# Kernel tuning notes

Hardware: AMD Instinct MI355X
Metric: run time of the kernel (lower is better)

Reference implementation:

```python
import jax, jax.numpy as jnp
import numpy as np

B, T, D = 1, 2048, 1024
HQ, HKV, HD = 16, 4, 64
G = HQ // HKV
E, TOPK, F = 8, 2, 2752
LB = 0.01
SCALE = HD ** -0.5


def setup_inputs() -> dict:
    key = jax.random.key(0)
    ks = jax.random.split(key, 12)
    s = 0.02
    return {
        "x": jax.random.normal(ks[0], (B, T, D), jnp.float32),
        "g1": jnp.ones((D,), jnp.float32),
        "g2": jnp.ones((D,), jnp.float32),
        "wq": jax.random.normal(ks[1], (D, HQ * HD), jnp.float32) * s,
        "wk": jax.random.normal(ks[2], (D, HKV * HD), jnp.float32) * s,
        "wv": jax.random.normal(ks[3], (D, HKV * HD), jnp.float32) * s,
        "wo": jax.random.normal(ks[4], (D, D), jnp.float32) * s,
        "gate_w": jax.random.normal(ks[5], (D, E), jnp.float32) * s,
        "we_gate": jax.random.normal(ks[6], (E, D, F), jnp.float32) * s,
        "we_up": jax.random.normal(ks[7], (E, D, F), jnp.float32) * s,
        "we_down": jax.random.normal(ks[8], (E, F, D), jnp.float32) * s,
    }


def _rmsnorm(x, g, eps=1e-6):
    return x * g * jax.lax.rsqrt(jnp.mean(x * x, axis=-1, keepdims=True) + eps)


def _rope(q, k):
    # q: [B,HQ,T,HD], k: [B,HKV,T,HD]; standard rotate-half RoPE
    pos = jnp.arange(T, dtype=jnp.float32)
    inv_freq = 1.0 / (10000.0 ** (jnp.arange(0, HD, 2, dtype=jnp.float32) / HD))
    ang = pos[:, None] * inv_freq[None, :]                  # [T, HD/2]
    cos = jnp.concatenate([jnp.cos(ang), jnp.cos(ang)], -1)  # [T, HD]
    sin = jnp.concatenate([jnp.sin(ang), jnp.sin(ang)], -1)

    def rot_half(x):
        x1, x2 = jnp.split(x, 2, axis=-1)
        return jnp.concatenate([-x2, x1], axis=-1)

    def apply(x):
        return x * cos + rot_half(x) * sin
    return apply(q), apply(k)


def _attention(x, g1, wq, wk, wv, wo):
    h = _rmsnorm(x, g1)
    q = (h @ wq).reshape(B, T, HQ, HD).transpose(0, 2, 1, 3)   # [B,HQ,T,HD]
    k = (h @ wk).reshape(B, T, HKV, HD).transpose(0, 2, 1, 3)  # [B,HKV,T,HD]
    v = (h @ wv).reshape(B, T, HKV, HD).transpose(0, 2, 1, 3)
    q, k = _rope(q, k)
    qg = q.reshape(B, HKV, G, T, HD)
    # grouped scores without materializing repeated K/V
    scores = jnp.einsum('bkgtd,bksd->bkgts', qg, k) * SCALE     # [B,HKV,G,T,T]
    causal = jnp.tril(jnp.ones((T, T), bool))
    scores = jnp.where(causal, scores, jnp.float32(-jnp.inf))
    w = jax.nn.softmax(scores, axis=-1)
    o = jnp.einsum('bkgts,bksd->bkgtd', w, v)                  # [B,HKV,G,T,HD]
    o = o.reshape(B, HQ, T, HD).transpose(0, 2, 1, 3).reshape(B, T, D)
    return o @ wo


def _moe(x, g2, gate_w, we_gate, we_up, we_down):
    h = _rmsnorm(x, g2).reshape(B * T, D)                      # [N,D]
    N = B * T
    logits = h @ gate_w                                        # [N,E]
    probs = jax.nn.softmax(logits, axis=-1)
    topv, topi = jax.lax.top_k(probs, TOPK)                    # [N,TOPK]
    topv = topv / (topv.sum(-1, keepdims=True) + 1e-8)
    # dense combine weights [N,E]: same math as masked per-expert dispatch
    combine = jnp.zeros((N, E), h.dtype).at[jnp.arange(N)[:, None], topi].add(topv)
    gh = jnp.einsum('nd,edf->enf', h, we_gate)
    up = jnp.einsum('nd,edf->enf', h, we_up)
    y = jnp.einsum('enf,efd->end', jax.nn.silu(gh) * up, we_down)
    out = jnp.einsum('end,ne->nd', y, combine).reshape(B, T, D)
    # load-balancing aux loss
    frac = jnp.zeros((E,), probs.dtype).at[topi.reshape(-1)].add(1.0) / (N * TOPK)
    load = probs.mean(axis=0)
    aux = LB * E * jnp.sum(frac * load)
    return out, aux


def reference(x, g1, g2, wq, wk, wv, wo, gate_w, we_gate, we_up, we_down):
    x = x + _attention(x, g1, wq, wk, wv, wo)
    moe_out, aux = _moe(x, g2, gate_w, we_gate, we_up, we_down)
    x = x + moe_out
    return x, aux
```

## Files before the change

kernel.cpp:

```cpp
#include <hip/hip_runtime.h>
#include <cstdint>

typedef __attribute__((ext_vector_type(8))) short short8;
typedef __attribute__((ext_vector_type(4))) float floatx4;
typedef __attribute__((ext_vector_type(4))) unsigned short ushort4v;
typedef unsigned short ushort;

#define T_LEN 2048
#define D_DIM 1024
#define HQn 16
#define HKVn 4
#define NE 8
#define FF 2752
#define NTOK 2048
#define NSLOT 4096
#define ATT_SCALE 0.125f
#define GATE_TPB 16

__device__ inline ushort f2bf(float f) {
  union { float f; unsigned int i; } v; v.f = f;
  unsigned int r = v.i + 0x7fffu + ((v.i >> 16) & 1u);
  return (ushort)(r >> 16);
}
__device__ inline float bf2f(ushort h) {
  union { unsigned int i; float f; } v; v.i = ((unsigned int)h) << 16;
  return v.f;
}
__device__ inline void split8(const float* v, short8& hi, short8& lo) {
#pragma unroll
  for (int i = 0; i < 8; i++) {
    ushort h = f2bf(v[i]);
    hi[i] = (short)h;
    lo[i] = (short)f2bf(v[i] - bf2f(h));
  }
}
__device__ inline floatx4 mfma16(short8 a, short8 b, floatx4 c) {
  return __builtin_amdgcn_mfma_f32_16x16x32_bf16(a, b, c, 0, 0, 0);
}
#define DMA16(g, l)                                                              \
  __builtin_amdgcn_global_load_lds((const __attribute__((address_space(1))) void*)(g), \
                                   (__attribute__((address_space(3))) void*)(l), 16, 0, 0)

__global__ __launch_bounds__(256) void k_cvtT(const float* __restrict__ src,
                                              ushort* __restrict__ dst, int R, int C) {
  __shared__ float tile[32][33];
  size_t sb = (size_t)blockIdx.z * R * C;
  const float* s = src + sb;
  ushort* d = dst + sb;
  int r0 = blockIdx.y * 32, c0 = blockIdx.x * 32;
  int tc = threadIdx.x & 31, tr = threadIdx.x >> 5;
#pragma unroll
  for (int i = 0; i < 4; i++)
    tile[tr + i * 8][tc] = s[(size_t)(r0 + tr + i * 8) * C + c0 + tc];
  __syncthreads();
#pragma unroll
  for (int i = 0; i < 4; i++) {
    int cc = tr + i * 8;
    d[(size_t)(c0 + cc) * R + r0 + tc] = f2bf(tile[tc][cc]);
  }
}

__global__ __launch_bounds__(256) void k_cvtT2(const float* __restrict__ src,
                                               ushort* __restrict__ dh,
                                               ushort* __restrict__ dl, int R, int C) {
  __shared__ float tile[32][33];
  int r0 = blockIdx.y * 32, c0 = blockIdx.x * 32;
  int tc = threadIdx.x & 31, tr = threadIdx.x >> 5;
#pragma unroll
  for (int i = 0; i < 4; i++)
    tile[tr + i * 8][tc] = src[(size_t)(r0 + tr + i * 8) * C + c0 + tc];
  __syncthreads();
#pragma unroll
  for (int i = 0; i < 4; i++) {
    int cc = tr + i * 8;
    float v = tile[tc][cc];
    ushort h = f2bf(v);
    dh[(size_t)(c0 + cc) * R + r0 + tc] = h;
    dl[(size_t)(c0 + cc) * R + r0 + tc] = f2bf(v - bf2f(h));
  }
}

__global__ __launch_bounds__(256) void k_rmsnorm2(const float* __restrict__ x,
                                                  const float* __restrict__ g,
                                                  ushort* __restrict__ oh,
                                                  ushort* __restrict__ ol) {
  int row = blockIdx.x;
  int t = threadIdx.x;
  const float4* x4 = (const float4*)(x + (size_t)row * D_DIM);
  float4 v = x4[t];
  float ss = v.x * v.x + v.y * v.y + v.z * v.z + v.w * v.w;
#pragma unroll
  for (int off = 32; off; off >>= 1) ss += __shfl_xor(ss, off, 64);
  __shared__ float red[4];
  if ((t & 63) == 0) red[t >> 6] = ss;
  __syncthreads();
  float tot = red[0] + red[1] + red[2] + red[3];
  float sc = rsqrtf(tot * (1.0f / D_DIM) + 1e-6f);
  const float4* g4 = (const float4*)g;
  float4 gv = g4[t];
  float vals[4] = {v.x * gv.x * sc, v.y * gv.y * sc, v.z * gv.z * sc, v.w * gv.w * sc};
  ushort4v h4, l4;
#pragma unroll
  for (int i = 0; i < 4; i++) {
    ushort h = f2bf(vals[i]);
    h4[i] = h;
    l4[i] = f2bf(vals[i] - bf2f(h));
  }
  *(ushort4v*)(oh + (size_t)row * D_DIM + t * 4) = h4;
  *(ushort4v*)(ol + (size_t)row * D_DIM + t * 4) = l4;
}

__global__ __launch_bounds__(256) void k_sgemm(const ushort* __restrict__ Ahg,
                                               const ushort* __restrict__ Alg,
                                               const ushort* __restrict__ Bhg,
                                               const ushort* __restrict__ Blg,
                                               float* __restrict__ C,
                                               const float* __restrict__ res,
                                               int N, int K) {
  __shared__ __align__(16) ushort Ah[2048], Al[2048], Bh[4096], Bl[4096];
  int tid = threadIdx.x;
  int m0 = blockIdx.y * 64, n0 = blockIdx.x * 128;
  int wave = tid >> 6, lane = tid & 63, quad = lane >> 4, l15 = lane & 15;
  int wm = (wave >> 1) * 32, wn = (wave & 1) * 64;
  floatx4 acc[2][4];
#pragma unroll
  for (int i = 0; i < 2; i++)
#pragma unroll
    for (int j = 0; j < 4; j++) acc[i][j] = (floatx4){0.f, 0.f, 0.f, 0.f};
  const ushort* src[6];
  ushort* dst[6];
  int srow = lane >> 2;
  int kc = ((lane & 3) ^ ((lane >> 3) & 3)) * 8;
#pragma unroll
  for (int j = 0; j < 6; j++) {
    int c = wave * 6 + j;
    if (c < 4) {
      src[j] = Ahg + (size_t)(m0 + c * 16 + srow) * K + kc;
      dst[j] = Ah + c * 512;
    } else if (c < 8) {
      src[j] = Alg + (size_t)(m0 + (c - 4) * 16 + srow) * K + kc;
      dst[j] = Al + (c - 4) * 512;
    } else if (c < 16) {
      src[j] = Bhg + (size_t)(n0 + (c - 8) * 16 + srow) * K + kc;
      dst[j] = Bh + (c - 8) * 512;
    } else {
      src[j] = Blg + (size_t)(n0 + (c - 16) * 16 + srow) * K + kc;
      dst[j] = Bl + (c - 16) * 512;
    }
  }
  for (int k0 = 0; k0 < K; k0 += 32) {
#pragma unroll
    for (int j = 0; j < 6; j++) DMA16(src[j] + k0, dst[j]);
    __syncthreads();
    short8 ah[2], al[2], bh[4], bl[4];
#pragma unroll
    for (int mt = 0; mt < 2; mt++) {
      int ar = wm + mt * 16 + l15;
      int sw = (quad ^ ((ar >> 1) & 3)) * 8;
      ah[mt] = *(short8*)&Ah[ar * 32 + sw];
      al[mt] = *(short8*)&Al[ar * 32 + sw];
    }
#pragma unroll
    for (int nt = 0; nt < 4; nt++) {
      int br = wn + nt * 16 + l15;
      int sw = (quad ^ ((br >> 1) & 3)) * 8;
      bh[nt] = *(short8*)&Bh[br * 32 + sw];
      bl[nt] = *(short8*)&Bl[br * 32 + sw];
    }
#pragma unroll
    for (int mt = 0; mt < 2; mt++)
#pragma unroll
      for (int nt = 0; nt < 4; nt++) {
        acc[mt][nt] = mfma16(ah[mt], bh[nt], acc[mt][nt]);
        acc[mt][nt] = mfma16(ah[mt], bl[nt], acc[mt][nt]);
        acc[mt][nt] = mfma16(al[mt], bh[nt], acc[mt][nt]);
      }
    __syncthreads();
  }
#pragma unroll
  for (int mt = 0; mt < 2; mt++) {
    int row = m0 + wm + mt * 16 + quad * 4;
#pragma unroll
    for (int nt = 0; nt < 4; nt++) {
      int col = n0 + wn + nt * 16 + l15;
#pragma unroll
      for (int r = 0; r < 4; r++) {
        float v = acc[mt][nt][r];
        if (res) v += res[(size_t)(row + r) * N + col];
        C[(size_t)(row + r) * N + col] = v;
      }
    }
  }
}

__global__ __launch_bounds__(256) void k_rope_cvt(const float* __restrict__ qkvf,
                                                  float* __restrict__ qbh,
                                                  float* __restrict__ kbh) {
  int t = blockIdx.x;
  const float* row = qkvf + (size_t)t * 1536;
  for (int it = threadIdx.x; it < (HQn + HKVn) * 32; it += 256) {
    int hh = it >> 5, i = it & 31;
    float inv = powf(10000.0f, -(float)i / 32.0f);
    float ang = (float)t * inv;
    float c = cosf(ang), s = sinf(ang);
    const float* p;
    float* dst;
    if (hh < HQn) {
      p = row + hh * 64;
      dst = qbh + ((size_t)hh * T_LEN + t) * 64;
    } else {
      int h2 = hh - HQn;
      p = row + 1024 + h2 * 64;
      dst = kbh + ((size_t)h2 * T_LEN + t) * 64;
    }
    float a = p[i], b = p[i + 32];
    dst[i] = a * c - b * s;
    dst[i + 32] = b * c + a * s;
  }
}

__global__ __launch_bounds__(256) void k_vT(const float* __restrict__ qkvf,
                                            float* __restrict__ vbt) {
  __shared__ float tile[32][33];
  int t0 = blockIdx.x * 32;
  int dh = blockIdx.y;
  int col0 = 1280 + dh * 32;
  int tc = threadIdx.x & 31, tr = threadIdx.x >> 5;
#pragma unroll
  for (int i = 0; i < 4; i++)
    tile[tr + i * 8][tc] = qkvf[(size_t)(t0 + tr + i * 8) * 1536 + col0 + tc];
  __syncthreads();
#pragma unroll
  for (int i = 0; i < 4; i++) {
    int dd = tr + i * 8;
    vbt[(size_t)(dh * 32 + dd) * T_LEN + t0 + tc] = tile[tc][dd];
  }
}

__global__ __launch_bounds__(256) void k_attn(const float* __restrict__ qbh,
                                              const float* __restrict__ kbh,
                                              const float* __restrict__ vbt,
                                              ushort* __restrict__ obh,
                                              ushort* __restrict__ obl) {
  __shared__ ushort Kh[64][72], Kl[64][72], Vh[64][72], Vl[64][72];
  __shared__ ushort Psh[4][16][72], Psl[4][16][72];
  int qh = blockIdx.y, kvh = qh >> 2;
  int r0 = blockIdx.x * 64;
  int tid = threadIdx.x, wave = tid >> 6, lane = tid & 63;
  int quad = lane >> 4, l15 = lane & 15;
#pragma unroll
  for (int it = 0; it < 2; it++) {
    int c = tid + it * 256;
    int row = c >> 3, col = (c & 7) * 8;
    float va[8];
    short8 h8, l8;
    const float* src = qbh + ((size_t)qh * T_LEN + r0 + row) * 64 + col;
    *(float4*)(va) = *(const float4*)(src);
    *(float4*)(va + 4) = *(const float4*)(src + 4);
    split8(va, h8, l8);
    *(short8*)&Kh[row][col] = h8;
    *(short8*)&Kl[row][col] = l8;
  }
  __syncthreads();
  short8 aqh0 = *(short8*)&Kh[wave * 16 + l15][quad * 8];
  short8 aqh1 = *(short8*)&Kh[wave * 16 + l15][32 + quad * 8];
  short8 aql0 = *(short8*)&Kl[wave * 16 + l15][quad * 8];
  short8 aql1 = *(short8*)&Kl[wave * 16 + l15][32 + quad * 8];
  floatx4 oacc[4];
#pragma unroll
  for (int nt = 0; nt < 4; nt++) oacc[nt] = (floatx4){0.f, 0.f, 0.f, 0.f};
  float mrun[4], lrun[4];
#pragma unroll
  for (int r = 0; r < 4; r++) { mrun[r] = -INFINITY; lrun[r] = 0.f; }
  int cq = r0 >> 6;
  for (int cc = 0; cc <= cq; cc++) {
    __syncthreads();
#pragma unroll
    for (int it = 0; it < 2; it++) {
      int c = tid + it * 256;
      int row = c >> 3, col = (c & 7) * 8;
      float va[8];
      short8 h8, l8;
      const float* ks = kbh + ((size_t)kvh * T_LEN + cc * 64 + row) * 64 + col;
      *(float4*)(va) = *(const float4*)(ks);
      *(float4*)(va + 4) = *(const float4*)(ks + 4);
      split8(va, h8, l8);
      *(short8*)&Kh[row][col] = h8;
      *(short8*)&Kl[row][col] = l8;
      const float* vs = vbt + ((size_t)(kvh * 64 + row)) * T_LEN + cc * 64 + col;
      *(float4*)(va) = *(const float4*)(vs);
      *(float4*)(va + 4) = *(const float4*)(vs + 4);
      split8(va, h8, l8);
      *(short8*)&Vh[row][col] = h8;
      *(short8*)&Vl[row][col] = l8;
    }
    __syncthreads();
    floatx4 s[4];
#pragma unroll
    for (int nt = 0; nt < 4; nt++) {
      short8 bh0 = *(short8*)&Kh[nt * 16 + l15][quad * 8];
      short8 bh1 = *(short8*)&Kh[nt * 16 + l15][32 + quad * 8];
      short8 bl0 = *(short8*)&Kl[nt * 16 + l15][quad * 8];
      short8 bl1 = *(short8*)&Kl[nt * 16 + l15][32 + quad * 8];
      floatx4 z = (floatx4){0.f, 0.f, 0.f, 0.f};
      z = mfma16(aqh0, bh0, z);
      z = mfma16(aqh1, bh1, z);
      z = mfma16(aqh0, bl0, z);
      z = mfma16(aqh1, bl1, z);
      z = mfma16(aql0, bh0, z);
      z = mfma16(aql1, bh1, z);
      s[nt] = z;
    }
    int rowg0 = r0 + wave * 16 + quad * 4;
#pragma unroll
    for (int nt = 0; nt < 4; nt++) {
      int colg = cc * 64 + nt * 16 + l15;
#pragma unroll
      for (int r = 0; r < 4; r++) {
        float v = s[nt][r] * ATT_SCALE;
        s[nt][r] = (colg > rowg0 + r) ? -INFINITY : v;
      }
    }
    float mnew[4], alpha[4], psum[4];
#pragma unroll
    for (int r = 0; r < 4; r++) {
      float mx = fmaxf(fmaxf(s[0][r], s[1][r]), fmaxf(s[2][r], s[3][r]));
#pragma unroll
      for (int off = 1; off < 16; off <<= 1) mx = fmaxf(mx, __shfl_xor(mx, off, 64));
      mnew[r] = fmaxf(mrun[r], mx);
      psum[r] = 0.f;
    }
#pragma unroll
    for (int nt = 0; nt < 4; nt++)
#pragma unroll
      for (int r = 0; r < 4; r++) {
        float p = __expf(s[nt][r] - mnew[r]);
        s[nt][r] = p;
        psum[r] += p;
      }
#pragma unroll
    for (int r = 0; r < 4; r++) {
      float ps = psum[r];
#pragma unroll
      for (int off = 1; off < 16; off <<= 1) ps += __shfl_xor(ps, off, 64);
      alpha[r] = __expf(mrun[r] - mnew[r]);
      lrun[r] = lrun[r] * alpha[r] + ps;
      mrun[r] = mnew[r];
    }
#pragma unroll
    for (int nt = 0; nt < 4; nt++)
#pragma unroll
      for (int r = 0; r < 4; r++) oacc[nt][r] *= alpha[r];
#pragma unroll
    for (int nt = 0; nt < 4; nt++)
#pragma unroll
      for (int r = 0; r < 4; r++) {
        float p = s[nt][r];
        ushort ph = f2bf(p);
        Psh[wave][quad * 4 + r][nt * 16 + l15] = ph;
        Psl[wave][quad * 4 + r][nt * 16 + l15] = f2bf(p - bf2f(ph));
      }
    short8 aph0 = *(short8*)&Psh[wave][l15][quad * 8];
    short8 aph1 = *(short8*)&Psh[wave][l15][32 + quad * 8];
    short8 apl0 = *(short8*)&Psl[wave][l15][quad * 8];
    short8 apl1 = *(short8*)&Psl[wave][l15][32 + quad * 8];
#pragma unroll
    for (int nt = 0; nt < 4; nt++) {
      short8 bvh0 = *(short8*)&Vh[nt * 16 + l15][quad * 8];
      short8 bvh1 = *(short8*)&Vh[nt * 16 + l15][32 + quad * 8];
      short8 bvl0 = *(short8*)&Vl[nt * 16 + l15][quad * 8];
      short8 bvl1 = *(short8*)&Vl[nt * 16 + l15][32 + quad * 8];
      oacc[nt] = mfma16(aph0, bvh0, oacc[nt]);
      oacc[nt] = mfma16(aph1, bvh1, oacc[nt]);
      oacc[nt] = mfma16(aph0, bvl0, oacc[nt]);
      oacc[nt] = mfma16(aph1, bvl1, oacc[nt]);
      oacc[nt] = mfma16(apl0, bvh0, oacc[nt]);
      oacc[nt] = mfma16(apl1, bvh1, oacc[nt]);
    }
  }
#pragma unroll
  for (int nt = 0; nt < 4; nt++)
#pragma unroll
    for (int r = 0; r < 4; r++) {
      int rowg = r0 + wave * 16 + quad * 4 + r;
      float v = oacc[nt][r] / lrun[r];
      ushort h = f2bf(v);
      size_t idx = (size_t)rowg * D_DIM + qh * 64 + nt * 16 + l15;
      obh[idx] = h;
      obl[idx] = f2bf(v - bf2f(h));
    }
}

__global__ __launch_bounds__(256) void k_gate(const float* __restrict__ x1,
                                              const float* __restrict__ g2,
                                              const float* __restrict__ gw,
                                              int* __restrict__ counts,
                                              int* __restrict__ ids,
                                              float* __restrict__ wts,
                                              float* __restrict__ load_sum) {
  __shared__ float lsum[NE];
  __shared__ int lcount[NE];
  __shared__ int lbase[NE];
  __shared__ int ltok[GATE_TPB * 2];
  __shared__ int lexp[GATE_TPB * 2];
  __shared__ float lwt[GATE_TPB * 2];
  int tid = threadIdx.x, wave = tid >> 6, lane = tid & 63;
  if (tid < NE) { lsum[tid] = 0.f; lcount[tid] = 0; }
  __syncthreads();
  int t0 = blockIdx.x * GATE_TPB;
#pragma unroll
  for (int tt = 0; tt < GATE_TPB / 4; tt++) {
    int tloc = tt * 4 + wave;
    int token = t0 + tloc;
    const float* xp = x1 + (size_t)token * D_DIM;
    float acc[NE] = {};
    float ss = 0.f;
    for (int d = lane; d < D_DIM; d += 64) {
      float xv = xp[d];
      ss += xv * xv;
      float hv = xv * g2[d];
#pragma unroll
      for (int e = 0; e < NE; e++) acc[e] += hv * gw[d * NE + e];
    }
#pragma unroll
    for (int off = 32; off; off >>= 1) ss += __shfl_xor(ss, off, 64);
#pragma unroll
    for (int e = 0; e < NE; e++)
#pragma unroll
      for (int off = 32; off; off >>= 1) acc[e] += __shfl_xor(acc[e], off, 64);
    if (lane == 0) {
      float sc = rsqrtf(ss * (1.0f / D_DIM) + 1e-6f);
      float mx = -1e30f;
#pragma unroll
      for (int e = 0; e < NE; e++) { acc[e] *= sc; mx = fmaxf(mx, acc[e]); }
      float p[NE], sum = 0.f;
#pragma unroll
      for (int e = 0; e < NE; e++) { p[e] = expf(acc[e] - mx); sum += p[e]; }
#pragma unroll
      for (int e = 0; e < NE; e++) p[e] /= sum;
      int i1 = 0;
#pragma unroll
      for (int e = 1; e < NE; e++) if (acc[e] > acc[i1]) i1 = e;
      int i2 = (i1 == 0) ? 1 : 0;
#pragma unroll
      for (int e = 0; e < NE; e++) if (e != i1 && acc[e] > acc[i2]) i2 = e;
      float denom = p[i1] + p[i2] + 1e-8f;
      int slot = tloc * 2;
      lexp[slot] = i1; ltok[slot] = token; lwt[slot] = p[i1] / denom;
      lexp[slot + 1] = i2; ltok[slot + 1] = token; lwt[slot + 1] = p[i2] / denom;
      atomicAdd(&lcount[i1], 1);
      atomicAdd(&lcount[i2], 1);
#pragma unroll
      for (int e = 0; e < NE; e++) atomicAdd(&lsum[e], p[e]);
    }
  }
  __syncthreads();
  if (tid < NE) {
    lbase[tid] = atomicAdd(&counts[tid], lcount[tid]);
    atomicAdd(&load_sum[tid], lsum[tid]);
    lcount[tid] = 0;
  }
  __syncthreads();
  if (tid < GATE_TPB * 2) {
    int e = lexp[tid];
    int off = atomicAdd(&lcount[e], 1);
    int pos = lbase[e] + off;
    ids[e * NTOK + pos] = ltok[tid];
    wts[e * NTOK + pos] = lwt[tid];
  }
}

__global__ void k_offsets(const int* __restrict__ counts, int* __restrict__ offsets) {
  if (threadIdx.x == 0 && blockIdx.x == 0) {
    int s = 0;
    for (int e = 0; e < NE; e++) { offsets[e] = s; s += counts[e]; }
  }
}

__global__ __launch_bounds__(256) void k_moe_gateup(const ushort* __restrict__ h,
                                                    const ushort* __restrict__ wgT,
                                                    const ushort* __restrict__ wuT,
                                                    const int* __restrict__ ids,
                                                    const float* __restrict__ wts,
                                                    const int* __restrict__ counts,
                                                    const int* __restrict__ offsets,
                                                    ushort* __restrict__ act) {
  int e = blockIdx.z;
  int cnt = counts[e];
  int m0 = blockIdx.y * 128;
  if (m0 >= cnt) return;
  int n0 = blockIdx.x * 64;
  __shared__ __align__(16) ushort As[4096], Bg[2048], Bu[2048];
  __shared__ int toks[128];
  __shared__ float wrow[128];
  int tid = threadIdx.x;
  if (tid < 128) {
    int mm = m0 + tid;
    toks[tid] = (mm < cnt) ? ids[e * NTOK + mm] : 0;
    wrow[tid] = (mm < cnt) ? wts[e * NTOK + mm] : 0.f;
  }
  __syncthreads();
  int wave = tid >> 6, lane = tid & 63, quad = lane >> 4, l15 = lane & 15;
  int wm = (wave >> 1) * 64, wn = (wave & 1) * 32;
  const ushort* Wg = wgT + (size_t)e * FF * D_DIM;
  const ushort* Wu = wuT + (size_t)e * FF * D_DIM;
  const ushort* src[4];
  ushort* dst[4];
  int srow = lane >> 2;
  int kc = ((lane & 3) ^ ((lane >> 3) & 3)) * 8;
#pragma unroll
  for (int j = 0; j < 4; j++) {
    int c = wave * 4 + j;
    if (c < 8) {
      src[j] = h + (size_t)toks[c * 16 + srow] * D_DIM + kc;
      dst[j] = As + c * 512;
    } else if (c < 12) {
      src[j] = Wg + (size_t)(n0 + (c - 8) * 16 + srow) * D_DIM + kc;
      dst[j] = Bg + (c - 8) * 512;
    } else {
      src[j] = Wu + (size_t)(n0 + (c - 12) * 16 + srow) * D_DIM + kc;
      dst[j] = Bu + (c - 12) * 512;
    }
  }
  floatx4 accg[4][2], accu[4][2];
#pragma unroll
  for (int i = 0; i < 4; i++)
#pragma unroll
    for (int j = 0; j < 2; j++) {
      accg[i][j] = (floatx4){0.f, 0.f, 0.f, 0.f};
      accu[i][j] = (floatx4){0.f, 0.f, 0.f, 0.f};
    }
  for (int k0 = 0; k0 < D_DIM; k0 += 32) {
#pragma unroll
    for (int j = 0; j < 4; j++) DMA16(src[j] + k0, dst[j]);
    __syncthreads();
    short8 aF[4], bgF[2], buF[2];
#pragma unroll
    for (int mt = 0; mt < 4; mt++) {
      int ar = wm + mt * 16 + l15;
      int sw = (quad ^ ((ar >> 1) & 3)) * 8;
      aF[mt] = *(short8*)&As[ar * 32 + sw];
    }
#pragma unroll
    for (int nt = 0; nt < 2; nt++) {
      int br = wn + nt * 16 + l15;
      int sw = (quad ^ ((br >> 1) & 3)) * 8;
      bgF[nt] = *(short8*)&Bg[br * 32 + sw];
      buF[nt] = *(short8*)&Bu[br * 32 + sw];
    }
#pragma unroll
    for (int mt = 0; mt < 4; mt++)
#pragma unroll
      for (int nt = 0; nt < 2; nt++) {
        accg[mt][nt] = mfma16(aF[mt], bgF[nt], accg[mt][nt]);
        accu[mt][nt] = mfma16(aF[mt], buF[nt], accu[mt][nt]);
      }
    __syncthreads();
  }
  int aoff = offsets[e];
#pragma unroll
  for (int mt = 0; mt < 4; mt++) {
    int mrow = wm + mt * 16 + quad * 4;
#pragma unroll
    for (int nt = 0; nt < 2; nt++) {
      int col = n0 + wn + nt * 16 + l15;
#pragma unroll
      for (int r = 0; r < 4; r++) {
        int ml = mrow + r;
        if (m0 + ml < cnt) {
          float g = accg[mt][nt][r];
          float u = accu[mt][nt][r];
          float sil = g / (1.f + __expf(-g));
          act[(size_t)(aoff + m0 + ml) * FF + col] = f2bf(sil * u * wrow[ml]);
        }
      }
    }
  }
}

__global__ __launch_bounds__(256) void k_moe_down(const ushort* __restrict__ act,
                                                  const ushort* __restrict__ wdT,
                                                  const int* __restrict__ ids,
                                                  const int* __restrict__ counts,
                                                  const int* __restrict__ offsets,
                                                  float* __restrict__ moe_acc) {
  int e = blockIdx.z & 7;
  int kh = blockIdx.z >> 3;
  int cnt = counts[e];
  int m0 = blockIdx.y * 128;
  if (m0 >= cnt) return;
  int n0 = blockIdx.x * 128;
  __shared__ __align__(16) ushort As[4096], Bs[4096];
  __shared__ int toks[128];
  int tid = threadIdx.x;
  if (tid < 128) {
    int mm = m0 + tid;
    toks[tid] = (mm < cnt) ? ids[e * NTOK + mm] : 0;
  }
  __syncthreads();
  int wave = tid >> 6, lane = tid & 63, quad = lane >> 4, l15 = lane & 15;
  int wm = (wave >> 1) * 64, wn = (wave & 1) * 64;
  int aoff = offsets[e];
  const ushort* Wd = wdT + (size_t)e * D_DIM * FF;
  const ushort* src[4];
  ushort* dst[4];
  int srow = lane >> 2;
  int kc = ((lane & 3) ^ ((lane >> 3) & 3)) * 8;
#pragma unroll
  for (int j = 0; j < 4; j++) {
    int c = wave * 4 + j;
    if (c < 8) {
      src[j] = act + (size_t)(aoff + m0 + c * 16 + srow) * FF + kc;
      dst[j] = As + c * 512;
    } else {
      src[j] = Wd + (size_t)(n0 + (c - 8) * 16 + srow) * FF + kc;
      dst[j] = Bs + (c - 8) * 512;
    }
  }
  floatx4 acc[4][4];
#pragma unroll
  for (int i = 0; i < 4; i++)
#pragma unroll
    for (int j = 0; j < 4; j++) acc[i][j] = (floatx4){0.f, 0.f, 0.f, 0.f};
  int kbeg = kh * 1376;
  for (int k0 = kbeg; k0 < kbeg + 1376; k0 += 32) {
#pragma unroll
    for (int j = 0; j < 4; j++) DMA16(src[j] + k0, dst[j]);
    __syncthreads();
    short8 aF[4], bF[4];
#pragma unroll
    for (int mt = 0; mt < 4; mt++) {
      int ar = wm + mt * 16 + l15;
      int sw = (quad ^ ((ar >> 1) & 3)) * 8;
      aF[mt] = *(short8*)&As[ar * 32 + sw];
    }
#pragma unroll
    for (int nt = 0; nt < 4; nt++) {
      int br = wn + nt * 16 + l15;
      int sw = (quad ^ ((br >> 1) & 3)) * 8;
      bF[nt] = *(short8*)&Bs[br * 32 + sw];
    }
#pragma unroll
    for (int mt = 0; mt < 4; mt++)
#pragma unroll
      for (int nt = 0; nt < 4; nt++) acc[mt][nt] = mfma16(aF[mt], bF[nt], acc[mt][nt]);
    __syncthreads();
  }
#pragma unroll
  for (int mt = 0; mt < 4; mt++) {
    int mrow = wm + mt * 16 + quad * 4;
#pragma unroll
    for (int nt = 0; nt < 4; nt++) {
      int col = n0 + wn + nt * 16 + l15;
#pragma unroll
      for (int r = 0; r < 4; r++) {
        int ml = mrow + r;
        if (m0 + ml < cnt)
          atomicAdd(&moe_acc[(size_t)toks[ml] * D_DIM + col], acc[mt][nt][r]);
      }
    }
  }
}

__global__ __launch_bounds__(256) void k_add(const float* __restrict__ a,
                                             const float* __restrict__ b,
                                             float* __restrict__ o) {
  int i = blockIdx.x * 256 + threadIdx.x;
  float4 va = ((const float4*)a)[i];
  float4 vb = ((const float4*)b)[i];
  float4 vo;
  vo.x = va.x + vb.x; vo.y = va.y + vb.y; vo.z = va.z + vb.z; vo.w = va.w + vb.w;
  ((float4*)o)[i] = vo;
}

__global__ void k_aux(const int* __restrict__ counts, const float* __restrict__ load_sum,
                      float* __restrict__ out_aux) {
  if (threadIdx.x == 0 && blockIdx.x == 0) {
    float s = 0.f;
    for (int e = 0; e < NE; e++)
      s += ((float)counts[e] / (float)NSLOT) * (load_sum[e] / (float)NTOK);
    *out_aux = 0.01f * (float)NE * s;
  }
}

extern "C" void kernel_launch(void* const* d_in, const int* in_sizes, int n_in,
                              void* d_out, int out_size, void* d_ws, size_t ws_size,
                              hipStream_t stream) {
  const float* x = (const float*)d_in[0];
  const float* g1 = (const float*)d_in[1];
  const float* g2 = (const float*)d_in[2];
  const float* wq = (const float*)d_in[3];
  const float* wk = (const float*)d_in[4];
  const float* wv = (const float*)d_in[5];
  const float* wo = (const float*)d_in[6];
  const float* gate_w = (const float*)d_in[7];
  const float* we_gate = (const float*)d_in[8];
  const float* we_up = (const float*)d_in[9];
  const float* we_down = (const float*)d_in[10];
  float* out = (float*)d_out;

  char* w = (char*)d_ws;
  size_t o = 0;
  auto alloc = [&](size_t bytes) -> char* {
    char* p = w + o;
    o = (o + bytes + 255) & ~(size_t)255;
    return p;
  };
  ushort* h1h = (ushort*)alloc((size_t)NTOK * D_DIM * 2);
  ushort* h1l = (ushort*)alloc((size_t)NTOK * D_DIM * 2);
  float* qkvf = (float*)alloc((size_t)NTOK * 1536 * 4);
  float* qbh = (float*)alloc((size_t)HQn * T_LEN * 64 * 4);
  float* kbh = (float*)alloc((size_t)HKVn * T_LEN * 64 * 4);
  float* vbt = (float*)alloc((size_t)HKVn * 64 * T_LEN * 4);
  ushort* obh = (ushort*)alloc((size_t)NTOK * D_DIM * 2);
  ushort* obl = (ushort*)alloc((size_t)NTOK * D_DIM * 2);
  float* x1 = (float*)alloc((size_t)NTOK * D_DIM * 4);
  float* moe_acc = (float*)alloc((size_t)NTOK * D_DIM * 4);
  ushort* act = (ushort*)alloc((size_t)(NSLOT + 128) * FF * 2);
  ushort* qkvwTh = (ushort*)alloc((size_t)1536 * 1024 * 2);
  ushort* qkvwTl = (ushort*)alloc((size_t)1536 * 1024 * 2);
  ushort* woTh = (ushort*)alloc((size_t)1024 * 1024 * 2);
  ushort* woTl = (ushort*)alloc((size_t)1024 * 1024 * 2);
  ushort* h2h = (ushort*)alloc((size_t)NTOK * D_DIM * 2);
  ushort* h2l = (ushort*)alloc((size_t)NTOK * D_DIM * 2);
  ushort* wgT = (ushort*)alloc((size_t)NE * FF * D_DIM * 2);
  ushort* wuT = (ushort*)alloc((size_t)NE * FF * D_DIM * 2);
  ushort* wdT = (ushort*)alloc((size_t)NE * D_DIM * FF * 2);
  int* counts = (int*)alloc(NE * 4);
  int* offsets = (int*)alloc(NE * 4);
  float* load_sum = (float*)alloc(NE * 4);
  int* ids = (int*)alloc((size_t)NE * NTOK * 4);
  float* wts = (float*)alloc((size_t)NE * NTOK * 4);

  hipMemsetAsync(moe_acc, 0, (size_t)NTOK * D_DIM * 4, stream);
  hipMemsetAsync(counts, 0, 768, stream);

  k_cvtT2<<<dim3(32, 32), 256, 0, stream>>>(wq, qkvwTh, qkvwTl, 1024, 1024);
  k_cvtT2<<<dim3(8, 32), 256, 0, stream>>>(wk, qkvwTh + (size_t)1024 * 1024,
                                           qkvwTl + (size_t)1024 * 1024, 1024, 256);
  k_cvtT2<<<dim3(8, 32), 256, 0, stream>>>(wv, qkvwTh + (size_t)1280 * 1024,
                                           qkvwTl + (size_t)1280 * 1024, 1024, 256);
  k_cvtT2<<<dim3(32, 32), 256, 0, stream>>>(wo, woTh, woTl, 1024, 1024);
  k_cvtT<<<dim3(86, 32, 8), 256, 0, stream>>>(we_gate, wgT, 1024, 2752);
  k_cvtT<<<dim3(86, 32, 8), 256, 0, stream>>>(we_up, wuT, 1024, 2752);
  k_cvtT<<<dim3(32, 86, 8), 256, 0, stream>>>(we_down, wdT, 2752, 1024);

  k_rmsnorm2<<<NTOK, 256, 0, stream>>>(x, g1, h1h, h1l);
  k_sgemm<<<dim3(12, 32), 256, 0, stream>>>(h1h, h1l, qkvwTh, qkvwTl, qkvf, nullptr,
                                            1536, 1024);
  k_rope_cvt<<<T_LEN, 256, 0, stream>>>(qkvf, qbh, kbh);
  k_vT<<<dim3(64, 8), 256, 0, stream>>>(qkvf, vbt);
  k_attn<<<dim3(32, 16), 256, 0, stream>>>(qbh, kbh, vbt, obh, obl);
  k_sgemm<<<dim3(8, 32), 256, 0, stream>>>(obh, obl, woTh, woTl, x1, x, 1024, 1024);

  k_rmsnorm2<<<NTOK, 256, 0, stream>>>(x1, g2, h2h, h2l);
  k_gate<<<NTOK / GATE_TPB, 256, 0, stream>>>(x1, g2, gate_w, counts, ids, wts, load_sum);
  k_offsets<<<1, 1, 0, stream>>>(counts, offsets);
  k_moe_gateup<<<dim3(43, 16, 8), 256, 0, stream>>>(h2h, wgT, wuT, ids, wts, counts,
                                                    offsets, act);
  k_moe_down<<<dim3(8, 16, 16), 256, 0, stream>>>(act, wdT, ids, counts, offsets, moe_acc);
  k_add<<<(NTOK * D_DIM) / (256 * 4), 256, 0, stream>>>(x1, moe_acc, out);
  k_aux<<<1, 1, 0, stream>>>(counts, load_sum, out + (size_t)NTOK * D_DIM);
}
```

Before: 755.0 us.

## Pre-split Q/K/V to bf16 hi/lo, DMA K/V tiles, pair causal tiles per block

RoPE and V-transpose kernels now write bf16 hi/lo pairs directly, so the attention kernel no longer converts fp32 to split bf16 on every K/V tile load. K/V tiles are copied into XOR-swizzled LDS with direct global-to-LDS transfers, and Q fragments are read straight from global memory. Each block now handles two query tiles (xt and 31-xt) to balance causal work, halving the grid. This trades more launch parallelism for balanced blocks and depends on DMA16 and the swizzle being correct.

```diff
diff --git a/kernel.cpp b/kernel.cpp
--- a/kernel.cpp
+++ b/kernel.cpp
@@ -194,8 +194,10 @@
 }
 
 __global__ __launch_bounds__(256) void k_rope_cvt(const float* __restrict__ qkvf,
-                                                  float* __restrict__ qbh,
-                                                  float* __restrict__ kbh) {
+                                                  ushort* __restrict__ qhi,
+                                                  ushort* __restrict__ qlo,
+                                                  ushort* __restrict__ khi,
+                                                  ushort* __restrict__ klo) {
   int t = blockIdx.x;
   const float* row = qkvf + (size_t)t * 1536;
   for (int it = threadIdx.x; it < (HQn + HKVn) * 32; it += 256) {
@@ -204,23 +206,33 @@
     float ang = (float)t * inv;
     float c = cosf(ang), s = sinf(ang);
     const float* p;
-    float* dst;
+    ushort *dh, *dl;
+    size_t base;
     if (hh < HQn) {
       p = row + hh * 64;
-      dst = qbh + ((size_t)hh * T_LEN + t) * 64;
+      base = ((size_t)hh * T_LEN + t) * 64;
+      dh = qhi; dl = qlo;
     } else {
       int h2 = hh - HQn;
       p = row + 1024 + h2 * 64;
-      dst = kbh + ((size_t)h2 * T_LEN + t) * 64;
+      base = ((size_t)h2 * T_LEN + t) * 64;
+      dh = khi; dl = klo;
     }
     float a = p[i], b = p[i + 32];
-    dst[i] = a * c - b * s;
-    dst[i + 32] = b * c + a * s;
+    float v0 = a * c - b * s;
+    float v1 = b * c + a * s;
+    ushort h0 = f2bf(v0);
+    dh[base + i] = h0;
+    dl[base + i] = f2bf(v0 - bf2f(h0));
+    ushort h1 = f2bf(v1);
+    dh[base + i + 32] = h1;
+    dl[base + i + 32] = f2bf(v1 - bf2f(h1));
   }
 }
 
 __global__ __launch_bounds__(256) void k_vT(const float* __restrict__ qkvf,
-                                            float* __restrict__ vbt) {
+                                            ushort* __restrict__ vbth,
+                                            ushort* __restrict__ vbtl) {
   __shared__ float tile[32][33];
   int t0 = blockIdx.x * 32;
   int dh = blockIdx.y;
@@ -233,162 +245,165 @@
 #pragma unroll
   for (int i = 0; i < 4; i++) {
     int dd = tr + i * 8;
-    vbt[(size_t)(dh * 32 + dd) * T_LEN + t0 + tc] = tile[tc][dd];
-  }
-}
-
-__global__ __launch_bounds__(256) void k_attn(const float* __restrict__ qbh,
-                                              const float* __restrict__ kbh,
-                                              const float* __restrict__ vbt,
+    float v = tile[tc][dd];
+    ushort h = f2bf(v);
+    size_t idx = (size_t)(dh * 32 + dd) * T_LEN + t0 + tc;
+    vbth[idx] = h;
+    vbtl[idx] = f2bf(v - bf2f(h));
+  }
+}
+
+__global__ __launch_bounds__(256) void k_attn(const ushort* __restrict__ qhi,
+                                              const ushort* __restrict__ qlo,
+                                              const ushort* __restrict__ khi,
+                                              const ushort* __restrict__ klo,
+                                              const ushort* __restrict__ vbth,
+                                              const ushort* __restrict__ vbtl,
                                               ushort* __restrict__ obh,
                                               ushort* __restrict__ obl) {
-  __shared__ ushort Kh[64][72], Kl[64][72], Vh[64][72], Vl[64][72];
-  __shared__ ushort Psh[4][16][72], Psl[4][16][72];
+  __shared__ __align__(16) ushort Kh[4096], Kl[4096], Vh[4096], Vl[4096];
+  __shared__ ushort Psh[4 * 16 * 72], Psl[4 * 16 * 72];
   int qh = blockIdx.y, kvh = qh >> 2;
-  int r0 = blockIdx.x * 64;
   int tid = threadIdx.x, wave = tid >> 6, lane = tid & 63;
   int quad = lane >> 4, l15 = lane & 15;
-#pragma unroll
-  for (int it = 0; it < 2; it++) {
-    int c = tid + it * 256;
-    int row = c >> 3, col = (c & 7) * 8;
-    float va[8];
-    short8 h8, l8;
-    const float* src = qbh + ((size_t)qh * T_LEN + r0 + row) * 64 + col;
-    *(float4*)(va) = *(const float4*)(src);
-    *(float4*)(va + 4) = *(const float4*)(src + 4);
-    split8(va, h8, l8);
-    *(short8*)&Kh[row][col] = h8;
-    *(short8*)&Kl[row][col] = l8;
-  }
-  __syncthreads();
-  short8 aqh0 = *(short8*)&Kh[wave * 16 + l15][quad * 8];
-  short8 aqh1 = *(short8*)&Kh[wave * 16 + l15][32 + quad * 8];
-  short8 aql0 = *(short8*)&Kl[wave * 16 + l15][quad * 8];
-  short8 aql1 = *(short8*)&Kl[wave * 16 + l15][32 + quad * 8];
-  floatx4 oacc[4];
-#pragma unroll
-  for (int nt = 0; nt < 4; nt++) oacc[nt] = (floatx4){0.f, 0.f, 0.f, 0.f};
-  float mrun[4], lrun[4];
-#pragma unroll
-  for (int r = 0; r < 4; r++) { mrun[r] = -INFINITY; lrun[r] = 0.f; }
-  int cq = r0 >> 6;
-  for (int cc = 0; cc <= cq; cc++) {
-    __syncthreads();
-#pragma unroll
-    for (int it = 0; it < 2; it++) {
-      int c = tid + it * 256;
-      int row = c >> 3, col = (c & 7) * 8;
-      float va[8];
-      short8 h8, l8;
-      const float* ks = kbh + ((size_t)kvh * T_LEN + cc * 64 + row) * 64 + col;
-      *(float4*)(va) = *(const float4*)(ks);
-      *(float4*)(va + 4) = *(const float4*)(ks + 4);
-      split8(va, h8, l8);
-      *(short8*)&Kh[row][col] = h8;
-      *(short8*)&Kl[row][col] = l8;
-      const float* vs = vbt + ((size_t)(kvh * 64 + row)) * T_LEN + cc * 64 + col;
-      *(float4*)(va) = *(const float4*)(vs);
-      *(float4*)(va + 4) = *(const float4*)(vs + 4);
-      split8(va, h8, l8);
-      *(short8*)&Vh[row][col] = h8;
-      *(short8*)&Vl[row][col] = l8;
-    }
-    __syncthreads();
-    floatx4 s[4];
-#pragma unroll
-    for (int nt = 0; nt < 4; nt++) {
-      short8 bh0 = *(short8*)&Kh[nt * 16 + l15][quad * 8];
-      short8 bh1 = *(short8*)&Kh[nt * 16 + l15][32 + quad * 8];
-      short8 bl0 = *(short8*)&Kl[nt * 16 + l15][quad * 8];
-      short8 bl1 = *(short8*)&Kl[nt * 16 + l15][32 + quad * 8];
-      floatx4 z = (floatx4){0.f, 0.f, 0.f, 0.f};
-      z = mfma16(aqh0, bh0, z);
-      z = mfma16(aqh1, bh1, z);
-      z = mfma16(aqh0, bl0, z);
-      z = mfma16(aqh1, bl1, z);
-      z = mfma16(aql0, bh0, z);
-      z = mfma16(aql1, bh1, z);
-      s[nt] = z;
-    }
-    int rowg0 = r0 + wave * 16 + quad * 4;
-#pragma unroll
-    for (int nt = 0; nt < 4; nt++) {
-      int colg = cc * 64 + nt * 16 + l15;
+  int sx = l15 >> 1;
+  int rlb = lane >> 3;
+  int csb = (lane & 7) ^ (lane >> 4);
+#pragma unroll 1
+  for (int hf = 0; hf < 2; hf++) {
+    int xt = hf ? (31 - (int)blockIdx.x) : (int)blockIdx.x;
+    int r0 = xt * 64;
+    const ushort* qbh_ = qhi + ((size_t)qh * T_LEN + r0 + wave * 16 + l15) * 64;
+    const ushort* qbl_ = qlo + ((size_t)qh * T_LEN + r0 + wave * 16 + l15) * 64;
+    short8 aqh0 = *(const short8*)&qbh_[quad * 8];
+    short8 aqh1 = *(const short8*)&qbh_[32 + quad * 8];
+    short8 aql0 = *(const short8*)&qbl_[quad * 8];
+    short8 aql1 = *(const short8*)&qbl_[32 + quad * 8];
+    floatx4 oacc[4];
+#pragma unroll
+    for (int nt = 0; nt < 4; nt++) oacc[nt] = (floatx4){0.f, 0.f, 0.f, 0.f};
+    float mrun[4], lrun[4];
+#pragma unroll
+    for (int r = 0; r < 4; r++) { mrun[r] = -INFINITY; lrun[r] = 0.f; }
+    for (int cc = 0; cc <= xt; cc++) {
+      __syncthreads();
+      if (wave < 2) {
+        const ushort* G = (wave == 0) ? khi : klo;
+        ushort* L = (wave == 0) ? Kh : Kl;
+        size_t rbase = (size_t)kvh * T_LEN + cc * 64;
+#pragma unroll
+        for (int i = 0; i < 8; i++) {
+          int ch = csb ^ ((i & 1) * 4);
+          DMA16(G + (rbase + i * 8 + rlb) * 64 + ch * 8, L + i * 512);
+        }
+      } else {
+        const ushort* G = (wave == 2) ? vbth : vbtl;
+        ushort* L = (wave == 2) ? Vh : Vl;
+#pragma unroll
+        for (int i = 0; i < 8; i++) {
+          int ch = csb ^ ((i & 1) * 4);
+          DMA16(G + ((size_t)(kvh * 64 + i * 8 + rlb)) * T_LEN + cc * 64 + ch * 8,
+                L + i * 512);
+        }
+      }
+      __syncthreads();
+      floatx4 s[4];
+#pragma unroll
+      for (int nt = 0; nt < 4; nt++) {
+        int row = nt * 16 + l15;
+        short8 bh0 = *(short8*)&Kh[row * 64 + (quad ^ sx) * 8];
+        short8 bh1 = *(short8*)&Kh[row * 64 + ((4 + quad) ^ sx) * 8];
+        short8 bl0 = *(short8*)&Kl[row * 64 + (quad ^ sx) * 8];
+        short8 bl1 = *(short8*)&Kl[row * 64 + ((4 + quad) ^ sx) * 8];
+        floatx4 z = (floatx4){0.f, 0.f, 0.f, 0.f};
+        z = mfma16(aqh0, bh0, z);
+        z = mfma16(aqh1, bh1, z);
+        z = mfma16(aqh0, bl0, z);
+        z = mfma16(aqh1, bl1, z);
+        z = mfma16(aql0, bh0, z);
+        z = mfma16(aql1, bh1, z);
+        s[nt] = z;
+      }
+      int rowg0 = r0 + wave * 16 + quad * 4;
+#pragma unroll
+      for (int nt = 0; nt < 4; nt++) {
+        int colg = cc * 64 + nt * 16 + l15;
+#pragma unroll
+        for (int r = 0; r < 4; r++) {
+          float v = s[nt][r] * ATT_SCALE;
+          s[nt][r] = (colg > rowg0 + r) ? -INFINITY : v;
+        }
+      }
+      float mnew[4], alpha[4], psum[4];
 #pragma unroll
       for (int r = 0; r < 4; r++) {
-        float v = s[nt][r] * ATT_SCALE;
-        s[nt][r] = (colg > rowg0 + r) ? -INFINITY : v;
-      }
-    }
-    float mnew[4], alpha[4], psum[4];
-#pragma unroll
-    for (int r = 0; r < 4; r++) {
-      float mx = fmaxf(fmaxf(s[0][r], s[1][r]), fmaxf(s[2][r], s[3][r]));
-#pragma unroll
-      for (int off = 1; off < 16; off <<= 1) mx = fmaxf(mx, __shfl_xor(mx, off, 64));
-      mnew[r] = fmaxf(mrun[r], mx);
-      psum[r] = 0.f;
+        float mx = fmaxf(fmaxf(s[0][r], s[1][r]), fmaxf(s[2][r], s[3][r]));
+#pragma unroll
+        for (int off = 1; off < 16; off <<= 1) mx = fmaxf(mx, __shfl_xor(mx, off, 64));
+        mnew[r] = fmaxf(mrun[r], mx);
+        psum[r] = 0.f;
+      }
+#pragma unroll
+      for (int nt = 0; nt < 4; nt++)
+#pragma unroll
+        for (int r = 0; r < 4; r++) {
+          float p = __expf(s[nt][r] - mnew[r]);
+          s[nt][r] = p;
+          psum[r] += p;
+        }
+#pragma unroll
+      for (int r = 0; r < 4; r++) {
+        float ps = psum[r];
+#pragma unroll
+        for (int off = 1; off < 16; off <<= 1) ps += __shfl_xor(ps, off, 64);
+        alpha[r] = __expf(mrun[r] - mnew[r]);
+        lrun[r] = lrun[r] * alpha[r] + ps;
+        mrun[r] = mnew[r];
+      }
+#pragma unroll
+      for (int nt = 0; nt < 4; nt++)
+#pragma unroll
+        for (int r = 0; r < 4; r++) oacc[nt][r] *= alpha[r];
+#pragma unroll
+      for (int nt = 0; nt < 4; nt++)
+#pragma unroll
+        for (int r = 0; r < 4; r++) {
+          float p = s[nt][r];
+          ushort ph = f2bf(p);
+          Psh[wave * 1152 + (quad * 4 + r) * 72 + nt * 16 + l15] = ph;
+          Psl[wave * 1152 + (quad * 4 + r) * 72 + nt * 16 + l15] = f2bf(p - bf2f(ph));
+        }
+      short8 aph0 = *(short8*)&Psh[wave * 1152 + l15 * 72 + quad * 8];
+      short8 aph1 = *(short8*)&Psh[wave * 1152 + l15 * 72 + 32 + quad * 8];
+      short8 apl0 = *(short8*)&Psl[wave * 1152 + l15 * 72 + quad * 8];
+      short8 apl1 = *(short8*)&Psl[wave * 1152 + l15 * 72 + 32 + quad * 8];
+#pragma unroll
+      for (int nt = 0; nt < 4; nt++) {
+        int row = nt * 16 + l15;
+        short8 bvh0 = *(short8*)&Vh[row * 64 + (quad ^ sx) * 8];
+        short8 bvh1 = *(short8*)&Vh[row * 64 + ((4 + quad) ^ sx) * 8];
+        short8 bvl0 = *(short8*)&Vl[row * 64 + (quad ^ sx) * 8];
+        short8 bvl1 = *(short8*)&Vl[row * 64 + ((4 + quad) ^ sx) * 8];
+        oacc[nt] = mfma16(aph0, bvh0, oacc[nt]);
+        oacc[nt] = mfma16(aph1, bvh1, oacc[nt]);
+        oacc[nt] = mfma16(aph0, bvl0, oacc[nt]);
+        oacc[nt] = mfma16(aph1, bvl1, oacc[nt]);
+        oacc[nt] = mfma16(apl0, bvh0, oacc[nt]);
+        oacc[nt] = mfma16(apl1, bvh1, oacc[nt]);
+      }
     }
 #pragma unroll
     for (int nt = 0; nt < 4; nt++)
 #pragma unroll
       for (int r = 0; r < 4; r++) {
-        float p = __expf(s[nt][r] - mnew[r]);
-        s[nt][r] = p;
-        psum[r] += p;
-      }
-#pragma unroll
-    for (int r = 0; r < 4; r++) {
-      float ps = psum[r];
-#pragma unroll
-      for (int off = 1; off < 16; off <<= 1) ps += __shfl_xor(ps, off, 64);
-      alpha[r] = __expf(mrun[r] - mnew[r]);
-      lrun[r] = lrun[r] * alpha[r] + ps;
-      mrun[r] = mnew[r];
-    }
-#pragma unroll
-    for (int nt = 0; nt < 4; nt++)
-#pragma unroll
-      for (int r = 0; r < 4; r++) oacc[nt][r] *= alpha[r];
-#pragma unroll
-    for (int nt = 0; nt < 4; nt++)
-#pragma unroll
-      for (int r = 0; r < 4; r++) {
-        float p = s[nt][r];
-        ushort ph = f2bf(p);
-        Psh[wave][quad * 4 + r][nt * 16 + l15] = ph;
-        Psl[wave][quad * 4 + r][nt * 16 + l15] = f2bf(p - bf2f(ph));
-      }
-    short8 aph0 = *(short8*)&Psh[wave][l15][quad * 8];
-    short8 aph1 = *(short8*)&Psh[wave][l15][32 + quad * 8];
-    short8 apl0 = *(short8*)&Psl[wave][l15][quad * 8];
-    short8 apl1 = *(short8*)&Psl[wave][l15][32 + quad * 8];
-#pragma unroll
-    for (int nt = 0; nt < 4; nt++) {
-      short8 bvh0 = *(short8*)&Vh[nt * 16 + l15][quad * 8];
-      short8 bvh1 = *(short8*)&Vh[nt * 16 + l15][32 + quad * 8];
-      short8 bvl0 = *(short8*)&Vl[nt * 16 + l15][quad * 8];
-      short8 bvl1 = *(short8*)&Vl[nt * 16 + l15][32 + quad * 8];
-      oacc[nt] = mfma16(aph0, bvh0, oacc[nt]);
-      oacc[nt] = mfma16(aph1, bvh1, oacc[nt]);
-      oacc[nt] = mfma16(aph0, bvl0, oacc[nt]);
-      oacc[nt] = mfma16(aph1, bvl1, oacc[nt]);
-      oacc[nt] = mfma16(apl0, bvh0, oacc[nt]);
-      oacc[nt] = mfma16(apl1, bvh1, oacc[nt]);
-    }
-  }
-#pragma unroll
-  for (int nt = 0; nt < 4; nt++)
-#pragma unroll
-    for (int r = 0; r < 4; r++) {
-      int rowg = r0 + wave * 16 + quad * 4 + r;
-      float v = oacc[nt][r] / lrun[r];
-      ushort h = f2bf(v);
-      size_t idx = (size_t)rowg * D_DIM + qh * 64 + nt * 16 + l15;
-      obh[idx] = h;
-      obl[idx] = f2bf(v - bf2f(h));
-    }
+        int rowg = r0 + wave * 16 + quad * 4 + r;
+        float v = oacc[nt][r] / lrun[r];
+        ushort h = f2bf(v);
+        size_t idx = (size_t)rowg * D_DIM + qh * 64 + nt * 16 + l15;
+        obh[idx] = h;
+        obl[idx] = f2bf(v - bf2f(h));
+      }
+  }
 }
 
 __global__ __launch_bounds__(256) void k_gate(const float* __restrict__ x1,
@@ -709,9 +724,12 @@
   ushort* h1h = (ushort*)alloc((size_t)NTOK * D_DIM * 2);
   ushort* h1l = (ushort*)alloc((size_t)NTOK * D_DIM * 2);
   float* qkvf = (float*)alloc((size_t)NTOK * 1536 * 4);
-  float* qbh = (float*)alloc((size_t)HQn * T_LEN * 64 * 4);
-  float* kbh = (float*)alloc((size_t)HKVn * T_LEN * 64 * 4);
-  float* vbt = (float*)alloc((size_t)HKVn * 64 * T_LEN * 4);
+  ushort* qhi = (ushort*)alloc((size_t)HQn * T_LEN * 64 * 2);
+  ushort* qlo = (ushort*)alloc((size_t)HQn * T_LEN * 64 * 2);
+  ushort* khi = (ushort*)alloc((size_t)HKVn * T_LEN * 64 * 2);
+  ushort* klo = (ushort*)alloc((size_t)HKVn * T_LEN * 64 * 2);
+  ushort* vbth = (ushort*)alloc((size_t)HKVn * 64 * T_LEN * 2);
+  ushort* vbtl = (ushort*)alloc((size_t)HKVn * 64 * T_LEN * 2);
   ushort* obh = (ushort*)alloc((size_t)NTOK * D_DIM * 2);
   ushort* obl = (ushort*)alloc((size_t)NTOK * D_DIM * 2);
   float* x1 = (float*)alloc((size_t)NTOK * D_DIM * 4);
@@ -748,9 +766,9 @@
   k_rmsnorm2<<<NTOK, 256, 0, stream>>>(x, g1, h1h, h1l);
   k_sgemm<<<dim3(12, 32), 256, 0, stream>>>(h1h, h1l, qkvwTh, qkvwTl, qkvf, nullptr,
                                             1536, 1024);
-  k_rope_cvt<<<T_LEN, 256, 0, stream>>>(qkvf, qbh, kbh);
-  k_vT<<<dim3(64, 8), 256, 0, stream>>>(qkvf, vbt);
-  k_attn<<<dim3(32, 16), 256, 0, stream>>>(qbh, kbh, vbt, obh, obl);
+  k_rope_cvt<<<T_LEN, 256, 0, stream>>>(qkvf, qhi, qlo, khi, klo);
+  k_vT<<<dim3(64, 8), 256, 0, stream>>>(qkvf, vbth, vbtl);
+  k_attn<<<dim3(16, 16), 256, 0, stream>>>(qhi, qlo, khi, klo, vbth, vbtl, obh, obl);
   k_sgemm<<<dim3(8, 32), 256, 0, stream>>>(obh, obl, woTh, woTl, x1, x, 1024, 1024);
 
   k_rmsnorm2<<<NTOK, 256, 0, stream>>>(x1, g2, h2h, h2l);
```

Result: faster. 709.9 us (-6.0%).
